# Optimization experiments

Measured on AMD Instinct MI355X. Metric: run time of the kernel, lower is better.

Reference implementation:

```python
import jax, jax.numpy as jnp
import numpy as np

W_POSE, W_MATCH, W_EPI = 1.0, 0.5, 0.1
EPS = 1e-8


def setup_inputs() -> dict:
    key = jax.random.key(0)
    ks = jax.random.split(key, 8)
    B, N, M = 16, 1024, 1024
    R_pred = jax.random.normal(ks[0], (B, 3, 3), dtype=jnp.float32)
    t_pred = jax.random.normal(ks[1], (B, 3), dtype=jnp.float32)
    R_gt = jax.random.normal(ks[2], (B, 3, 3), dtype=jnp.float32)
    t_gt = jax.random.normal(ks[3], (B, 3), dtype=jnp.float32)
    # realistic invertible camera intrinsics + small randn perturbation
    K_base = jnp.array([[500.0, 0.0, 320.0], [0.0, 500.0, 240.0], [0.0, 0.0, 1.0]], dtype=jnp.float32)
    K = K_base[None] + 0.01 * jax.random.normal(ks[4], (B, 3, 3), dtype=jnp.float32)
    kp1 = jax.random.normal(ks[5], (B, N, 2), dtype=jnp.float32)
    kp2 = jax.random.normal(ks[6], (B, N, 2), dtype=jnp.float32)
    matches = jax.random.uniform(ks[7], (B, N, M), dtype=jnp.float32)
    return {"R_pred": R_pred, "t_pred": t_pred, "R_gt": R_gt, "t_gt": t_gt,
            "K": K, "kp1": kp1, "kp2": kp2, "matches": matches}


def _homo(pts):
    # [B,N,2] -> [B,N,3]
    return jnp.concatenate([pts, jnp.ones(pts.shape[:-1] + (1,), pts.dtype)], axis=-1)


def _masked_weighted_mean(errors, matches):
    # samples with <3 surviving pairs are skipped (mirrors torch.where + skip).
    thr = jnp.max(matches, axis=(1, 2), keepdims=True) * 0.1
    mask = matches > thr
    w = jnp.where(mask, matches, 0.0)
    count = jnp.sum(mask, axis=(1, 2))
    valid = count >= 3
    per_b = jnp.sum(errors * w, axis=(1, 2)) / (jnp.sum(w, axis=(1, 2)) + EPS)
    per_b = jnp.where(valid, per_b, 0.0)
    n_valid = jnp.sum(valid)
    return jnp.where(n_valid > 0, jnp.sum(per_b) / jnp.maximum(n_valid, 1), 0.0)


def _fundamental(R, t, K):
    t_n = t / jnp.linalg.norm(t, axis=1, keepdims=True)  # F.normalize p=2 dim=1
    z = jnp.zeros_like(t_n[:, 0])
    t_skew = jnp.stack([
        jnp.stack([z, -t_n[:, 2], t_n[:, 1]], axis=-1),
        jnp.stack([t_n[:, 2], z, -t_n[:, 0]], axis=-1),
        jnp.stack([-t_n[:, 1], t_n[:, 0], z], axis=-1),
    ], axis=1)  # [B,3,3]
    E = jnp.einsum('bij,bjk->bik', t_skew, R)
    K_inv = jnp.linalg.inv(K)
    return jnp.einsum('bji,bjk,bkl->bil', K_inv, E, K_inv)  # K_inv^T E K_inv


def reference(R_pred, t_pred, R_gt, t_gt, K, kp1, kp2, matches):
    # rotation loss
    trace = jnp.einsum('bij,bij->b', R_pred, R_gt)  # trace(R_pred @ R_gt^T)
    geodesic = jnp.clip((trace - 1.0) / 2.0, -1.0 + 1e-7, 1.0 - 1e-7)
    rot_loss = jnp.mean(1.0 - geodesic)
    # translation loss
    t_gt_n = t_gt / jnp.linalg.norm(t_gt, axis=1, keepdims=True)
    trans_loss = jnp.mean(1.0 - jnp.sum(t_pred * t_gt_n, axis=1))
    pose_loss = rot_loss + trans_loss

    pts1_h = _homo(kp1)  # [B,N,3]
    pts2_h = _homo(kp2)  # [B,M,3]

    # correspondence loss: transformed pts1 by R_gt, error vs every kp2 -> [B,N,M]
    T = jnp.einsum('bij,bnj->bni', R_gt, pts1_h)[..., :2]  # [B,N,2]
    diff = kp2[:, None, :, :] - T[:, :, None, :]           # [B,N,M,2]
    corr_err = jnp.linalg.norm(diff, axis=-1)              # [B,N,M]
    match_loss = _masked_weighted_mean(corr_err, matches)

    # epipolar loss: |pts2_h[j]^T F pts1_h[i]| -> [B,N,M] indexed (i,j)
    F_mat = _fundamental(R_gt, t_gt, K)
    A = jnp.einsum('bmk,bkl->bml', pts2_h, F_mat)          # [B,M,3]
    epi_err = jnp.abs(jnp.einsum('bml,bnl->bnm', A, pts1_h))
    epi_loss = _masked_weighted_mean(epi_err, matches)

    total = W_POSE * pose_loss + W_MATCH * match_loss + W_EPI * epi_loss
    return total
```

## Files before the change

kernel.cpp:

```cpp
#include <hip/hip_runtime.h>

#define B 16
#define N 1024
#define M 1024
#define TN 16
#define BPB (N / TN)
#define NBLK (B * BPB)
#define C2 64

#define WS_CNTR  0
#define WS_RES   16
#define WS_PMAX  256
#define WS_BCNT  1536
#define WS_PACC  2560
#define WS_BAND  6656

#define NEG_INF (-3.402823466e+38f)

__device__ __forceinline__ void compute_F(const float* __restrict__ Rgp,
                                          const float* __restrict__ tg,
                                          const float* __restrict__ Km,
                                          float* F)
{
    float m00=Km[0], m01=Km[1], m02=Km[2];
    float m10=Km[3], m11=Km[4], m12=Km[5];
    float m20=Km[6], m21=Km[7], m22=Km[8];
    float c00 =  (m11*m22 - m12*m21), c01 = -(m10*m22 - m12*m20), c02 =  (m10*m21 - m11*m20);
    float c10 = -(m01*m22 - m02*m21), c11 =  (m00*m22 - m02*m20), c12 = -(m00*m21 - m01*m20);
    float c20 =  (m01*m12 - m02*m11), c21 = -(m00*m12 - m02*m10), c22 =  (m00*m11 - m01*m10);
    float id  = 1.f / (m00*c00 + m01*c01 + m02*c02);
    float Ki00 = c00*id, Ki01 = c10*id, Ki02 = c20*id;
    float Ki10 = c01*id, Ki11 = c11*id, Ki12 = c21*id;
    float Ki20 = c02*id, Ki21 = c12*id, Ki22 = c22*id;
    float inr = rsqrtf(tg[0]*tg[0] + tg[1]*tg[1] + tg[2]*tg[2]);
    float tx = tg[0]*inr, ty = tg[1]*inr, tz = tg[2]*inr;
    float Rg0=Rgp[0],Rg1=Rgp[1],Rg2=Rgp[2],Rg3=Rgp[3],Rg4=Rgp[4],Rg5=Rgp[5],Rg6=Rgp[6],Rg7=Rgp[7],Rg8=Rgp[8];
    float E00=-tz*Rg3+ty*Rg6, E01=-tz*Rg4+ty*Rg7, E02=-tz*Rg5+ty*Rg8;
    float E10= tz*Rg0-tx*Rg6, E11= tz*Rg1-tx*Rg7, E12= tz*Rg2-tx*Rg8;
    float E20=-ty*Rg0+tx*Rg3, E21=-ty*Rg1+tx*Rg4, E22=-ty*Rg2+tx*Rg5;
    float T00=E00*Ki00+E01*Ki10+E02*Ki20, T01=E00*Ki01+E01*Ki11+E02*Ki21, T02=E00*Ki02+E01*Ki12+E02*Ki22;
    float T10=E10*Ki00+E11*Ki10+E12*Ki20, T11=E10*Ki01+E11*Ki11+E12*Ki21, T12=E10*Ki02+E11*Ki12+E12*Ki22;
    float T20=E20*Ki00+E21*Ki10+E22*Ki20, T21=E20*Ki01+E21*Ki11+E22*Ki21, T22=E20*Ki02+E21*Ki12+E22*Ki22;
    F[0]=Ki00*T00+Ki10*T10+Ki20*T20; F[1]=Ki00*T01+Ki10*T11+Ki20*T21; F[2]=Ki00*T02+Ki10*T12+Ki20*T22;
    F[3]=Ki01*T00+Ki11*T10+Ki21*T20; F[4]=Ki01*T01+Ki11*T11+Ki21*T21; F[5]=Ki01*T02+Ki11*T12+Ki21*T22;
    F[6]=Ki02*T00+Ki12*T10+Ki22*T20; F[7]=Ki02*T01+Ki12*T11+Ki22*T21; F[8]=Ki02*T02+Ki12*T12+Ki22*T22;
}

__launch_bounds__(256, 4)
__global__ void k1_fused(const float* __restrict__ matches,
                         const float* __restrict__ R_gt, const float* __restrict__ t_gt,
                         const float* __restrict__ Kin,
                         const float* __restrict__ kp1,  const float* __restrict__ kp2,
                         float* __restrict__ ws)
{
    const int bid = blockIdx.x;
    const int b = bid >> 6;
    const int row0 = (bid & 63) * TN;
    const int t = threadIdx.x;
    const int lane = t & 63, wv = t >> 6;
    if (bid == 0 && t == 0) ((unsigned int*)ws)[WS_CNTR] = 0u;

    __shared__ float4 sTP[TN];
    __shared__ float  sm[4];
    __shared__ float4 paccL[4];
    __shared__ int    wtot[4];

    const float4* m4 = (const float4*)matches + ((long)b * N + row0) * (M/4) + t;
    float4 d[TN];
    #pragma unroll
    for (int n = 0; n < TN; ++n) d[n] = m4[n * (M/4)];

    const float* Rgp = R_gt + b * 9;
    if (t < TN) {
        float2 p = ((const float2*)kp1)[(long)b * N + row0 + t];
        sTP[t] = make_float4(Rgp[0]*p.x + Rgp[1]*p.y + Rgp[2],
                             Rgp[3]*p.x + Rgp[4]*p.y + Rgp[5], p.x, p.y);
    }

    float F[9];
    compute_F(Rgp, t_gt + b*3, Kin + b*9, F);
    const float4* kp2v = (const float4*)(kp2 + (long)b * M * 2);
    float4 q0 = kp2v[2*t], q1 = kp2v[2*t + 1];
    float k2x[4] = {q0.x, q0.z, q1.x, q1.z};
    float k2y[4] = {q0.y, q0.w, q1.y, q1.w};
    float A0[4], A1[4], A2[4];
    #pragma unroll
    for (int j = 0; j < 4; ++j) {
        A0[j] = k2x[j]*F[0] + k2y[j]*F[3] + F[6];
        A1[j] = k2x[j]*F[1] + k2y[j]*F[4] + F[7];
        A2[j] = k2x[j]*F[2] + k2y[j]*F[5] + F[8];
    }

    float v = NEG_INF;
    #pragma unroll
    for (int n = 0; n < TN; ++n)
        v = fmaxf(v, fmaxf(fmaxf(d[n].x, d[n].y), fmaxf(d[n].z, d[n].w)));
    #pragma unroll
    for (int off = 32; off; off >>= 1) v = fmaxf(v, __shfl_down(v, off));
    if (lane == 0) sm[wv] = v;
    __syncthreads();

    float bmax = fmaxf(fmaxf(sm[0], sm[1]), fmaxf(sm[2], sm[3]));
    if (t == 0) ws[WS_PMAX + bid] = bmax;
    float thr_b = 0.1f * bmax;
    float cap_b = 1.01f * thr_b;

    float s_w = 0.f, s_c = 0.f, s_e = 0.f, s_n = 0.f;
    int bcnt = 0;
    #pragma unroll
    for (int n = 0; n < TN; ++n) {
        float4 tp = sTP[n];
        float mv[4] = {d[n].x, d[n].y, d[n].z, d[n].w};
        #pragma unroll
        for (int j = 0; j < 4; ++j) {
            float w = mv[j];
            bool pass = w > thr_b;
            float ww = pass ? w : 0.f;
            s_n += pass ? 1.f : 0.f;
            bcnt += (pass && w <= cap_b) ? 1 : 0;
            float dx = k2x[j] - tp.x, dy = k2y[j] - tp.y;
            float ce = sqrtf(dx*dx + dy*dy);
            float ee = fabsf(A0[j]*tp.z + A1[j]*tp.w + A2[j]);
            s_w += ww; s_c += ce*ww; s_e += ee*ww;
        }
    }
    #pragma unroll
    for (int off = 32; off; off >>= 1) {
        s_w += __shfl_down(s_w, off);
        s_c += __shfl_down(s_c, off);
        s_e += __shfl_down(s_e, off);
        s_n += __shfl_down(s_n, off);
    }
    int incl = bcnt;
    #pragma unroll
    for (int off = 1; off < 64; off <<= 1) {
        int y = __shfl_up(incl, off);
        if (lane >= off) incl += y;
    }
    if (lane == 0)  paccL[wv] = make_float4(s_w, s_c, s_e, s_n);
    if (lane == 63) wtot[wv] = incl;
    __syncthreads();
    if (t == 0) {
        float4 r = paccL[0];
        #pragma unroll
        for (int i = 1; i < 4; ++i) { r.x += paccL[i].x; r.y += paccL[i].y; r.z += paccL[i].z; r.w += paccL[i].w; }
        ((float4*)(ws + WS_PACC))[bid] = r;
    }
    int pos = incl - bcnt;
    #pragma unroll
    for (int k = 0; k < 4; ++k) if (k < wv) pos += wtot[k];
    int total = wtot[0] + wtot[1] + wtot[2] + wtot[3];
    if (t == 0) ((unsigned int*)ws)[WS_BCNT + bid] = (unsigned int)total;

    if (total > 0 && total <= C2) {
        float* band = ws + WS_BAND + (long)bid * (C2 * 3);
        #pragma unroll
        for (int n = 0; n < TN; ++n) {
            float4 tp = sTP[n];
            float mv[4] = {d[n].x, d[n].y, d[n].z, d[n].w};
            #pragma unroll
            for (int j = 0; j < 4; ++j) {
                float w = mv[j];
                if (w > thr_b && w <= cap_b) {
                    float dx = k2x[j] - tp.x, dy = k2y[j] - tp.y;
                    float ce = sqrtf(dx*dx + dy*dy);
                    float ee = fabsf(A0[j]*tp.z + A1[j]*tp.w + A2[j]);
                    band[pos*3 + 0] = w;
                    band[pos*3 + 1] = ce * w;
                    band[pos*3 + 2] = ee * w;
                    ++pos;
                }
            }
        }
    }
}

__launch_bounds__(256)
__global__ void k2_perb(const float* __restrict__ matches,
                        const float* __restrict__ R_pred, const float* __restrict__ t_pred,
                        const float* __restrict__ R_gt,   const float* __restrict__ t_gt,
                        const float* __restrict__ Kin,
                        const float* __restrict__ kp1,    const float* __restrict__ kp2,
                        float* __restrict__ ws, float* __restrict__ out)
{
    const int b = blockIdx.x;
    const int t = threadIdx.x;
    const int lane = t & 63, wv = t >> 6;

    __shared__ float        sPM[BPB];
    __shared__ unsigned int sBC[BPB];
    __shared__ int          sBad[BPB];
    __shared__ float        sThr;
    __shared__ float        sAcc4[4];
    __shared__ float        sPose;
    __shared__ int          sFlag[BPB];
    __shared__ int          sNFlag;
    __shared__ int          sLast;
    __shared__ float4       sTP[TN];

    if (t == 64) sNFlag = 0;

    if (t == 0) {
        const float* Rp = R_pred + b * 9;
        const float* Rq = R_gt   + b * 9;
        float trace = 0.f;
        #pragma unroll
        for (int i = 0; i < 9; ++i) trace += Rp[i] * Rq[i];
        float geo = fminf(fmaxf((trace - 1.f) * 0.5f, -1.f + 1e-7f), 1.f - 1e-7f);
        const float* tq = t_gt   + b * 3;
        const float* tp = t_pred + b * 3;
        float in2 = rsqrtf(tq[0]*tq[0] + tq[1]*tq[1] + tq[2]*tq[2]);
        float dotp = (tp[0]*tq[0] + tp[1]*tq[1] + tp[2]*tq[2]) * in2;
        sPose = (1.f - geo) + (1.f - dotp);
    }

    float4 myPacc = make_float4(0.f, 0.f, 0.f, 0.f);
    if (t < BPB) {
        sPM[t] = ws[WS_PMAX + b*BPB + t];
        sBC[t] = ((const unsigned int*)ws)[WS_BCNT + b*BPB + t];
        myPacc = ((const float4*)(ws + WS_PACC))[b*BPB + t];
    }
    __syncthreads();

    if (t < 64) {
        float v = sPM[t];
        #pragma unroll
        for (int off = 32; off; off >>= 1) v = fmaxf(v, __shfl_down(v, off));
        if (t == 0) sThr = 0.1f * v;
    }
    __syncthreads();
    const float thr = sThr;

    if (t < BPB) {
        bool bad = (sBC[t] > (unsigned)C2) || (thr > 1.01f * (0.1f * sPM[t]));
        sBad[t] = bad ? 1 : 0;
        if (bad) {
            int i = atomicAdd(&sNFlag, 1);
            sFlag[i] = t;
            myPacc = make_float4(0.f, 0.f, 0.f, 0.f);
        }
    }
    #pragma unroll
    for (int off = 32; off; off >>= 1) {
        myPacc.x += __shfl_down(myPacc.x, off);
        myPacc.y += __shfl_down(myPacc.y, off);
        myPacc.z += __shfl_down(myPacc.z, off);
        myPacc.w += __shfl_down(myPacc.w, off);
    }
    if (t == 0) {
        sAcc4[0] = myPacc.x; sAcc4[1] = myPacc.y;
        sAcc4[2] = myPacc.z; sAcc4[3] = myPacc.w;
    }
    __syncthreads();

    {
        int bidl = t >> 2;
        int q    = t & 3;
        float s0 = 0.f, s1 = 0.f, s2 = 0.f, s3 = 0.f;
        if (!sBad[bidl]) {
            unsigned int bc = sBC[bidl];
            const float* band = ws + WS_BAND + (long)(b*BPB + bidl) * (C2 * 3);
            for (unsigned int k = q; k < bc; k += 4) {
                float w = band[k*3 + 0];
                if (!(w > thr)) { s0 += w; s1 += band[k*3 + 1]; s2 += band[k*3 + 2]; s3 += 1.f; }
            }
        }
        #pragma unroll
        for (int off = 32; off; off >>= 1) {
            s0 += __shfl_down(s0, off);
            s1 += __shfl_down(s1, off);
            s2 += __shfl_down(s2, off);
            s3 += __shfl_down(s3, off);
        }
        if (lane == 0) {
            atomicAdd(&sAcc4[0], -s0);
            atomicAdd(&sAcc4[1], -s1);
            atomicAdd(&sAcc4[2], -s2);
            atomicAdd(&sAcc4[3], -s3);
        }
    }
    __syncthreads();

    const int nflag = sNFlag;
    for (int f = 0; f < nflag; ++f) {
        __syncthreads();
        int rrow0 = sFlag[f] * TN;
        const float* Rgp = R_gt + b * 9;
        if (t < TN) {
            float2 p = ((const float2*)kp1)[(long)b * N + rrow0 + t];
            sTP[t] = make_float4(Rgp[0]*p.x + Rgp[1]*p.y + Rgp[2],
                                 Rgp[3]*p.x + Rgp[4]*p.y + Rgp[5], p.x, p.y);
        }
        float F[9];
        compute_F(Rgp, t_gt + b*3, Kin + b*9, F);
        const float4* kp2v = (const float4*)(kp2 + (long)b * M * 2);
        float4 q0 = kp2v[2*t], q1 = kp2v[2*t + 1];
        float k2x[4] = {q0.x, q0.z, q1.x, q1.z};
        float k2y[4] = {q0.y, q0.w, q1.y, q1.w};
        float A0[4], A1[4], A2[4];
        #pragma unroll
        for (int j = 0; j < 4; ++j) {
            A0[j] = k2x[j]*F[0] + k2y[j]*F[3] + F[6];
            A1[j] = k2x[j]*F[1] + k2y[j]*F[4] + F[7];
            A2[j] = k2x[j]*F[2] + k2y[j]*F[5] + F[8];
        }
        const float4* m4 = (const float4*)matches + ((long)b * N + rrow0) * (M/4) + t;
        float4 d[TN];
        #pragma unroll
        for (int n = 0; n < TN; ++n) d[n] = m4[n * (M/4)];
        __syncthreads();
        float s_w = 0.f, s_c = 0.f, s_e = 0.f, s_n = 0.f;
        #pragma unroll
        for (int n = 0; n < TN; ++n) {
            float4 tp = sTP[n];
            float mv[4] = {d[n].x, d[n].y, d[n].z, d[n].w};
            #pragma unroll
            for (int j = 0; j < 4; ++j) {
                float w = mv[j];
                bool pass = w > thr;
                float ww = pass ? w : 0.f;
                s_n += pass ? 1.f : 0.f;
                float dx = k2x[j] - tp.x, dy = k2y[j] - tp.y;
                float ce = sqrtf(dx*dx + dy*dy);
                float ee = fabsf(A0[j]*tp.z + A1[j]*tp.w + A2[j]);
                s_w += ww; s_c += ce*ww; s_e += ee*ww;
            }
        }
        #pragma unroll
        for (int off = 32; off; off >>= 1) {
            s_w += __shfl_down(s_w, off);
            s_c += __shfl_down(s_c, off);
            s_e += __shfl_down(s_e, off);
            s_n += __shfl_down(s_n, off);
        }
        if (lane == 0) {
            atomicAdd(&sAcc4[0], s_w);
            atomicAdd(&sAcc4[1], s_c);
            atomicAdd(&sAcc4[2], s_e);
            atomicAdd(&sAcc4[3], s_n);
        }
        __syncthreads();
    }
    __syncthreads();

    if (t == 0) {
        float* res = ws + WS_RES + b * 8;
        res[0] = sAcc4[0]; res[1] = sAcc4[1]; res[2] = sAcc4[2]; res[3] = sAcc4[3];
        res[4] = sPose;
        __threadfence();
        unsigned int old = atomicAdd(((unsigned int*)ws) + WS_CNTR, 1u);
        sLast = (old == (unsigned int)(B - 1)) ? 1 : 0;
    }
    __syncthreads();
    if (!sLast) return;
    __threadfence();

    if (wv == 0) {
        float po = 0.f, msv = 0.f, esv = 0.f, nvv = 0.f;
        if (lane < B) {
            const float* res = ws + WS_RES + lane * 8;
            float sw = res[0], sc = res[1], se = res[2], cn = res[3];
            po = res[4];
            if (cn >= 3.f) {
                nvv = 1.f;
                msv = sc / (sw + 1e-8f);
                esv = se / (sw + 1e-8f);
            }
        }
        #pragma unroll
        for (int off = 8; off; off >>= 1) {
            po  += __shfl_down(po,  off);
            msv += __shfl_down(msv, off);
            esv += __shfl_down(esv, off);
            nvv += __shfl_down(nvv, off);
        }
        if (lane == 0) {
            float match = nvv > 0.f ? msv / nvv : 0.f;
            float epi   = nvv > 0.f ? esv / nvv : 0.f;
            out[0] = po * (1.f / (float)B) + 0.5f * match + 0.1f * epi;
        }
    }
}

extern "C" void kernel_launch(void* const* d_in, const int* in_sizes, int n_in,
                              void* d_out, int out_size, void* d_ws, size_t ws_size,
                              hipStream_t stream) {
    const float* R_pred  = (const float*)d_in[0];
    const float* t_pred  = (const float*)d_in[1];
    const float* R_gt    = (const float*)d_in[2];
    const float* t_gt    = (const float*)d_in[3];
    const float* K       = (const float*)d_in[4];
    const float* kp1     = (const float*)d_in[5];
    const float* kp2     = (const float*)d_in[6];
    const float* matches = (const float*)d_in[7];
    float* out = (float*)d_out;
    float* ws  = (float*)d_ws;

    k1_fused<<<NBLK, 256, 0, stream>>>(matches, R_gt, t_gt, K, kp1, kp2, ws);
    k2_perb <<<B,    256, 0, stream>>>(matches, R_pred, t_pred, R_gt, t_gt, K, kp1, kp2, ws, out);
}
```

Before: 44.80 us.

## Shrink row tile to four rows per block to launch more blocks

Reduces rows per k1 block from 16 to 4, raising the block count from 1024 to 4096 and cutting per-thread register-held match data. The per-batch band capacity is halved and the workspace offsets are recomputed. k2 is rewritten so all 256 threads each handle one partial block, with cross-wave reductions through shared memory for the max and the partial accumulators. The intent is better latency hiding and occupancy in the streaming pass. In exchange there is more partial-result traffic and more blocks marked bad, which fall back to a slower recompute path.

```diff
diff --git a/kernel.cpp b/kernel.cpp
--- a/kernel.cpp
+++ b/kernel.cpp
@@ -3,17 +3,17 @@
 #define B 16
 #define N 1024
 #define M 1024
-#define TN 16
+#define TN 4
 #define BPB (N / TN)
 #define NBLK (B * BPB)
-#define C2 64
+#define C2 32
 
 #define WS_CNTR  0
 #define WS_RES   16
 #define WS_PMAX  256
-#define WS_BCNT  1536
-#define WS_PACC  2560
-#define WS_BAND  6656
+#define WS_BCNT  4352
+#define WS_PACC  8448
+#define WS_BAND  24832
 
 #define NEG_INF (-3.402823466e+38f)
 
@@ -54,8 +54,8 @@
                          float* __restrict__ ws)
 {
     const int bid = blockIdx.x;
-    const int b = bid >> 6;
-    const int row0 = (bid & 63) * TN;
+    const int b = bid >> 8;
+    const int row0 = (bid & 255) * TN;
     const int t = threadIdx.x;
     const int lane = t & 63, wv = t >> 6;
     if (bid == 0 && t == 0) ((unsigned int*)ws)[WS_CNTR] = 0u;
@@ -190,7 +190,9 @@
     __shared__ float        sPM[BPB];
     __shared__ unsigned int sBC[BPB];
     __shared__ int          sBad[BPB];
+    __shared__ float        sm4[4];
     __shared__ float        sThr;
+    __shared__ float4       sPacc[4];
     __shared__ float        sAcc4[4];
     __shared__ float        sPose;
     __shared__ int          sFlag[BPB];
@@ -214,24 +216,24 @@
         sPose = (1.f - geo) + (1.f - dotp);
     }
 
-    float4 myPacc = make_float4(0.f, 0.f, 0.f, 0.f);
-    if (t < BPB) {
-        sPM[t] = ws[WS_PMAX + b*BPB + t];
-        sBC[t] = ((const unsigned int*)ws)[WS_BCNT + b*BPB + t];
-        myPacc = ((const float4*)(ws + WS_PACC))[b*BPB + t];
-    }
-    __syncthreads();
-
-    if (t < 64) {
+    float4 myPacc;
+    sPM[t] = ws[WS_PMAX + b*BPB + t];
+    sBC[t] = ((const unsigned int*)ws)[WS_BCNT + b*BPB + t];
+    myPacc = ((const float4*)(ws + WS_PACC))[b*BPB + t];
+    __syncthreads();
+
+    {
         float v = sPM[t];
         #pragma unroll
         for (int off = 32; off; off >>= 1) v = fmaxf(v, __shfl_down(v, off));
-        if (t == 0) sThr = 0.1f * v;
-    }
+        if (lane == 0) sm4[wv] = v;
+    }
+    __syncthreads();
+    if (t == 0) sThr = 0.1f * fmaxf(fmaxf(sm4[0], sm4[1]), fmaxf(sm4[2], sm4[3]));
     __syncthreads();
     const float thr = sThr;
 
-    if (t < BPB) {
+    {
         bool bad = (sBC[t] > (unsigned)C2) || (thr > 1.01f * (0.1f * sPM[t]));
         sBad[t] = bad ? 1 : 0;
         if (bad) {
@@ -247,20 +249,22 @@
         myPacc.z += __shfl_down(myPacc.z, off);
         myPacc.w += __shfl_down(myPacc.w, off);
     }
+    if (lane == 0) sPacc[wv] = myPacc;
+    __syncthreads();
     if (t == 0) {
-        sAcc4[0] = myPacc.x; sAcc4[1] = myPacc.y;
-        sAcc4[2] = myPacc.z; sAcc4[3] = myPacc.w;
+        sAcc4[0] = sPacc[0].x + sPacc[1].x + sPacc[2].x + sPacc[3].x;
+        sAcc4[1] = sPacc[0].y + sPacc[1].y + sPacc[2].y + sPacc[3].y;
+        sAcc4[2] = sPacc[0].z + sPacc[1].z + sPacc[2].z + sPacc[3].z;
+        sAcc4[3] = sPacc[0].w + sPacc[1].w + sPacc[2].w + sPacc[3].w;
     }
     __syncthreads();
 
     {
-        int bidl = t >> 2;
-        int q    = t & 3;
         float s0 = 0.f, s1 = 0.f, s2 = 0.f, s3 = 0.f;
-        if (!sBad[bidl]) {
-            unsigned int bc = sBC[bidl];
-            const float* band = ws + WS_BAND + (long)(b*BPB + bidl) * (C2 * 3);
-            for (unsigned int k = q; k < bc; k += 4) {
+        if (!sBad[t]) {
+            unsigned int bc = sBC[t];
+            const float* band = ws + WS_BAND + (long)(b*BPB + t) * (C2 * 3);
+            for (unsigned int k = 0; k < bc; ++k) {
                 float w = band[k*3 + 0];
                 if (!(w > thr)) { s0 += w; s1 += band[k*3 + 1]; s2 += band[k*3 + 2]; s3 += 1.f; }
             }
```

Result: faster. 40.02 us (-10.7%).
